# Kernel tuning notes

Measured on AMD Instinct MI355X. Metric: run time of the kernel, lower is better.

The kernel has to match this reference:

```python
import jax, jax.numpy as jnp
import numpy as np

H = 1024        # hidden_size
E = 8           # num_experts
K = 2           # top_k
FF = 4 * H      # expert hidden dim
B, S = 2, 2048


def setup_inputs() -> dict:
    key = jax.random.key(0)
    ks = jax.random.split(key, 7)
    scale = 0.02
    x = jax.random.normal(ks[0], (B, S, H), dtype=jnp.float32)
    Wg = jax.random.normal(ks[1], (H, E), dtype=jnp.float32) * scale
    bg = jnp.zeros((E,), dtype=jnp.float32)
    W1 = jax.random.normal(ks[2], (E, H, FF), dtype=jnp.float32) * scale
    b1 = jnp.zeros((E, FF), dtype=jnp.float32)
    W2 = jax.random.normal(ks[3], (E, FF, H), dtype=jnp.float32) * scale
    b2 = jnp.zeros((E, H), dtype=jnp.float32)
    return {"x": x, "Wg": Wg, "bg": bg, "W1": W1, "b1": b1, "W2": W2, "b2": b2}


def reference(x, Wg, bg, W1, b1, W2, b2):
    b, s, h = x.shape
    xf = x.reshape(-1, h)                                  # [T, H]
    T = xf.shape[0]
    # gating: softmax -> top-k -> renormalize
    probs = jax.nn.softmax(xf @ Wg + bg, axis=-1)          # [T, E]
    vals, idx = jax.lax.top_k(probs, K)                    # [T, K]
    vals = vals / jnp.sum(vals, axis=-1, keepdims=True)
    # dense combine weights: zero for non-selected experts (equivalent math)
    combine = jnp.zeros((T, E), dtype=x.dtype)
    combine = combine.at[jnp.arange(T)[:, None], idx].set(vals)  # [T, E]
    # all-expert FFN (GEMM-dominated), combined with sparse gate weights
    hmid = jax.nn.gelu(jnp.einsum('th,ehf->tef', xf, W1) + b1, approximate=False)  # [T,E,FF]
    y = jnp.einsum('tef,efh->teh', hmid, W2) + b2          # [T, E, H]
    out = jnp.einsum('te,teh->th', combine, y)             # [T, H]
    return out.reshape(b, s, h)
```

## Files before the change

### kernel.cpp

```cpp
#include <hip/hip_runtime.h>
#include <hip/hip_bf16.h>
#include <math.h>

#define T_TOK  4096
#define H_DIM  1024
#define E_NUM  8
#define FF_DIM 4096
#define KSEL   2
#define SLOTS  (T_TOK*KSEL)
#define SLOTS_PAD (SLOTS + 256)
#define BM 128
#define MAXTILES 72

typedef __attribute__((ext_vector_type(8))) short s16x8;
typedef __attribute__((ext_vector_type(8))) unsigned short u16x8;
typedef __attribute__((ext_vector_type(4))) float f32x4;

typedef __attribute__((address_space(1))) const void global_cvoid;
typedef __attribute__((address_space(3))) void lds_void;

__device__ __forceinline__ unsigned short f2bf(float f){
  unsigned int u = __float_as_uint(f);
  u += 0x7fffu + ((u>>16)&1u);
  return (unsigned short)(u>>16);
}
__device__ __forceinline__ float bf2f(unsigned short h){
  return __uint_as_float(((unsigned int)h)<<16);
}

static constexpr size_t OFF_CNT   = 0;
static constexpr size_t OFF_IDX   = 1280;
static constexpr size_t OFF_POS   = OFF_IDX  + 32768;
static constexpr size_t OFF_WV    = OFF_POS  + 32768;
static constexpr size_t OFF_SLOT  = OFF_WV   + 32768;
static constexpr size_t OFF_WOF   = OFF_SLOT + 32768;
static constexpr size_t OFF_XG    = OFF_WOF  + 32768;
static constexpr size_t OFF_W1T   = OFF_XG  + (size_t)SLOTS_PAD*H_DIM*2;
static constexpr size_t OFF_W2T   = OFF_W1T + (size_t)E_NUM*H_DIM*FF_DIM*2;
static constexpr size_t OFF_MID   = OFF_W2T + (size_t)E_NUM*H_DIM*FF_DIM*2;
static constexpr size_t OFF_Y     = OFF_MID + (size_t)SLOTS_PAD*FF_DIM*2;

__global__ __launch_bounds__(256) void prep_kernel(
    const float* __restrict__ W1, unsigned short* __restrict__ W1t,
    const float* __restrict__ W2, unsigned short* __restrict__ W2t,
    const float* __restrict__ x, const float* __restrict__ Wg,
    const float* __restrict__ bg, int* __restrict__ cnt,
    int* __restrict__ idxp, int* __restrict__ posp, float* __restrict__ wvp)
{
  int id = blockIdx.x;
  if (id < 256){
    int lane = threadIdx.x & 63;
    int wv = threadIdx.x >> 6;
    for (int tt=0; tt<4; ++tt){
      int t = (id*4 + wv)*4 + tt;
      const float* xr = x + (size_t)t*H_DIM;
      float acc[E_NUM];
      #pragma unroll
      for (int e=0;e<E_NUM;e++) acc[e]=0.f;
      for (int i=0;i<H_DIM/64;i++){
        int h = i*64 + lane;
        float xv = xr[h];
        const float* wr_ = Wg + (size_t)h*E_NUM;
        #pragma unroll
        for (int e=0;e<E_NUM;e++) acc[e] += xv*wr_[e];
      }
      #pragma unroll
      for (int e=0;e<E_NUM;e++){
        #pragma unroll
        for (int off=32; off>0; off>>=1) acc[e] += __shfl_xor(acc[e], off);
      }
      if (lane==0){
        float l[E_NUM];
        #pragma unroll
        for (int e=0;e<E_NUM;e++) l[e] = acc[e] + bg[e];
        int i0 = 0;
        #pragma unroll
        for (int e=1;e<E_NUM;e++) if (l[e] > l[i0]) i0 = e;
        int i1 = (i0==0)?1:0;
        #pragma unroll
        for (int e=0;e<E_NUM;e++) if (e!=i0 && l[e] > l[i1]) i1 = e;
        float p1 = expf(l[i1]-l[i0]);
        float s  = 1.f + p1;
        float w0 = 1.f/s, w1 = p1/s;
        int pos0 = atomicAdd(&cnt[i0],1);
        int pos1 = atomicAdd(&cnt[i1],1);
        idxp[t*2]=i0; idxp[t*2+1]=i1;
        posp[t*2]=pos0; posp[t*2+1]=pos1;
        wvp[t*2]=w0; wvp[t*2+1]=w1;
      }
    }
    return;
  }
  __shared__ float tile[64][65];
  int id2 = id - 256;
  const float* in; unsigned short* out; int R, C, cx, cy, e;
  if (id2 < 8192){
    e = id2 >> 10; int rem = id2 & 1023;
    cx = rem & 63; cy = rem >> 6;
    R = H_DIM; C = FF_DIM; in = W1; out = W1t;
  } else {
    int id3 = id2 - 8192;
    e = id3 >> 10; int rem = id3 & 1023;
    cx = rem & 15; cy = rem >> 4;
    R = FF_DIM; C = H_DIM; in = W2; out = W2t;
  }
  const float* inp = in + (size_t)e*R*C;
  unsigned short* op = out + (size_t)e*R*C;
  int c0 = cx*64, r0 = cy*64;
  int tx = threadIdx.x & 15, ty = threadIdx.x >> 4;
  #pragma unroll
  for (int i=0;i<4;i++){
    int r = i*16 + ty;
    float4 v = *(const float4*)(inp + (size_t)(r0+r)*C + c0 + tx*4);
    tile[r][tx*4+0]=v.x; tile[r][tx*4+1]=v.y; tile[r][tx*4+2]=v.z; tile[r][tx*4+3]=v.w;
  }
  __syncthreads();
  int wx = threadIdx.x & 7;
  int wcl = threadIdx.x >> 3;
  #pragma unroll
  for (int i=0;i<2;i++){
    int c = i*32 + wcl;
    u16x8 o;
    #pragma unroll
    for (int j=0;j<8;j++) o[j] = f2bf(tile[wx*8+j][c]);
    *(u16x8*)(op + (size_t)(c0+c)*R + r0 + wx*8) = o;
  }
}

__global__ __launch_bounds__(256) void route_gather_kernel(
    const float* __restrict__ x, const int* __restrict__ idxp,
    const int* __restrict__ posp, const float* __restrict__ wvp,
    const int* __restrict__ cnt,
    unsigned short* __restrict__ Xg, float* __restrict__ w_of,
    int* __restrict__ slot_of)
{
  int b = blockIdx.x;
  int t = b>>1;
  int e = idxp[b];
  int off = 0;
  #pragma unroll
  for (int i=0;i<E_NUM;i++) off += (i<e) ? cnt[i] : 0;
  int slot = off + posp[b];
  const float4* src = (const float4*)(x + (size_t)t*H_DIM);
  float4 v = src[threadIdx.x];
  ushort4 o;
  o.x=f2bf(v.x); o.y=f2bf(v.y); o.z=f2bf(v.z); o.w=f2bf(v.w);
  ((ushort4*)(Xg + (size_t)slot*H_DIM))[threadIdx.x] = o;
  if (threadIdx.x == 0){
    w_of[slot] = wvp[b];
    slot_of[b] = slot;
  }
}

#define GLDS(g, l) __builtin_amdgcn_global_load_lds((global_cvoid*)(g), (lds_void*)(l), 16, 0, 0)

template<int MODE>
__global__ __launch_bounds__(256, 4) void gemm128_kernel(
    const unsigned short* __restrict__ A,
    const unsigned short* __restrict__ Bt,
    const float* __restrict__ bias,
    unsigned short* __restrict__ Out,
    const int* __restrict__ cnt,
    const float* __restrict__ w_of,
    int N, int K, int cpcs)
{
  int L = blockIdx.x;
  int xcd = L & 7;
  int slot = L >> 3;
  int within = slot & 15;
  int chunk = ((slot >> 4) << 3) + xcd;
  int tb = chunk >> cpcs;
  int cb = chunk & ((1<<cpcs)-1);
  int tile_id = tb*4 + (within & 3);
  int col0 = (cb*4 + (within >> 2)) << 7;

  int e=0, row0=0, nv=0, acc_t=0, o=0, found=0;
  #pragma unroll
  for (int i=0;i<E_NUM;i++){
    int c = cnt[i];
    int nt = (c + BM-1) >> 7;
    if (!found && tile_id < acc_t + nt){
      int mt = tile_id - acc_t;
      e = i; row0 = o + mt*BM; nv = c - mt*BM; found = 1;
    }
    acc_t += nt; o += c;
  }
  if (!found) return;
  int nvalid = nv > BM ? BM : nv;
  const unsigned short* Be = Bt + (size_t)e*N*K;

  __shared__ unsigned short As[2][128*32];
  __shared__ unsigned short Bs[2][128*32];
  char* asb = (char*)&As[0][0];
  char* bsb = (char*)&Bs[0][0];

  int t = threadIdx.x;
  int wid = t>>6, lane = t&63;
  int wr = (wid>>1)*64, wc = (wid&1)*64;
  int fr = lane&15, fq = lane>>4;

  int srow = t>>2;
  int scl  = ((t&3) - ((t>>3)&3)) & 3;
  int sdst = wid*1024;

  const unsigned short* pA0 = A  + (size_t)(row0 + srow)*K      + scl*8;
  const unsigned short* pA1 = A  + (size_t)(row0 + 64 + srow)*K + scl*8;
  const unsigned short* pB0 = Be + (size_t)(col0 + srow)*K      + scl*8;
  const unsigned short* pB1 = Be + (size_t)(col0 + 64 + srow)*K + scl*8;

  auto stage = [&](int buf, int kelem){
    GLDS(pA0 + kelem, asb + buf*8192 + sdst);
    GLDS(pA1 + kelem, asb + buf*8192 + 4096 + sdst);
    GLDS(pB0 + kelem, bsb + buf*8192 + sdst);
    GLDS(pB1 + kelem, bsb + buf*8192 + 4096 + sdst);
  };

  int rd_sw = ((fq + ((fr>>1)&3)) & 3) << 4;

  f32x4 acc[4][4];
  #pragma unroll
  for (int i=0;i<4;i++)
    #pragma unroll
    for (int j=0;j<4;j++) acc[i][j] = (f32x4){0.f,0.f,0.f,0.f};

  int NT = K >> 5;
  stage(0, 0);
  stage(1, 32);
  for (int kt=0; kt<NT; ++kt){
    int cur = kt&1;
    if (kt+1 < NT) asm volatile("s_waitcnt vmcnt(4)" ::: "memory");
    else           asm volatile("s_waitcnt vmcnt(0)" ::: "memory");
    __builtin_amdgcn_s_barrier();
    asm volatile("" ::: "memory");

    s16x8 af[4], bfr[4];
    #pragma unroll
    for (int i=0;i<4;i++){
      af[i]  = *(const s16x8*)(asb + cur*8192 + (wr + i*16 + fr)*64 + rd_sw);
      bfr[i] = *(const s16x8*)(bsb + cur*8192 + (wc + i*16 + fr)*64 + rd_sw);
    }
    #pragma unroll
    for (int i=0;i<4;i++)
      #pragma unroll
      for (int j=0;j<4;j++)
        acc[i][j] = __builtin_amdgcn_mfma_f32_16x16x32_bf16(af[i], bfr[j], acc[i][j], 0,0,0);

    asm volatile("s_waitcnt lgkmcnt(0)" ::: "memory");
    __builtin_amdgcn_s_barrier();
    asm volatile("" ::: "memory");
    if (kt+2 < NT) stage(cur, (kt+2)*32);
  }

  float bias_v[4];
  #pragma unroll
  for (int j=0;j<4;j++) bias_v[j] = bias[(size_t)e*N + col0 + wc + j*16 + fr];
  #pragma unroll
  for (int i=0;i<4;i++){
    #pragma unroll
    for (int r=0;r<4;r++){
      int lrow = wr + i*16 + fq*4 + r;
      if (lrow < nvalid){
        int grow = row0 + lrow;
        float scale = (MODE==1) ? w_of[grow] : 0.f;
        #pragma unroll
        for (int j=0;j<4;j++){
          int col = col0 + wc + j*16 + fr;
          float v = acc[i][j][r] + bias_v[j];
          if (MODE==0){
            float u = v*(0.7978845608f + 0.0356774081f*v*v);
            float z = __expf(2.f*u);
            v = v - __fdividef(v, z + 1.f);
          } else {
            v *= scale;
          }
          Out[(size_t)grow*N + col] = f2bf(v);
        }
      }
    }
  }
}

__global__ __launch_bounds__(256) void combine_kernel(
    const unsigned short* __restrict__ y, const int* __restrict__ slot_of,
    float* __restrict__ out)
{
  int tok = blockIdx.x;
  int s0 = slot_of[tok*2], s1 = slot_of[tok*2+1];
  const ushort4* y0 = (const ushort4*)(y + (size_t)s0*H_DIM);
  const ushort4* y1 = (const ushort4*)(y + (size_t)s1*H_DIM);
  float4* o = (float4*)(out + (size_t)tok*H_DIM);
  ushort4 a = y0[threadIdx.x], b = y1[threadIdx.x];
  float4 r;
  r.x = bf2f(a.x)+bf2f(b.x);
  r.y = bf2f(a.y)+bf2f(b.y);
  r.z = bf2f(a.z)+bf2f(b.z);
  r.w = bf2f(a.w)+bf2f(b.w);
  o[threadIdx.x] = r;
}

extern "C" void kernel_launch(void* const* d_in, const int* in_sizes, int n_in,
                              void* d_out, int out_size, void* d_ws, size_t ws_size,
                              hipStream_t stream) {
  const float* x  = (const float*)d_in[0];
  const float* Wg = (const float*)d_in[1];
  const float* bg = (const float*)d_in[2];
  const float* W1 = (const float*)d_in[3];
  const float* b1 = (const float*)d_in[4];
  const float* W2 = (const float*)d_in[5];
  const float* b2 = (const float*)d_in[6];
  float* out = (float*)d_out;
  char* ws = (char*)d_ws;

  int*   cnt      = (int*)  (ws + OFF_CNT);
  int*   idxp     = (int*)  (ws + OFF_IDX);
  int*   posp     = (int*)  (ws + OFF_POS);
  float* wvp      = (float*)(ws + OFF_WV);
  int*   slot_of  = (int*)  (ws + OFF_SLOT);
  float* w_of     = (float*)(ws + OFF_WOF);
  unsigned short* Xg  = (unsigned short*)(ws + OFF_XG);
  unsigned short* W1t = (unsigned short*)(ws + OFF_W1T);
  unsigned short* W2t = (unsigned short*)(ws + OFF_W2T);
  unsigned short* mid = (unsigned short*)(ws + OFF_MID);
  unsigned short* y   = (unsigned short*)(ws + OFF_Y);

  hipMemsetAsync(ws + OFF_CNT, 0, 32, stream);

  prep_kernel<<<dim3(16640), 256, 0, stream>>>(
      W1, W1t, W2, W2t, x, Wg, bg, cnt, idxp, posp, wvp);
  route_gather_kernel<<<SLOTS, 256, 0, stream>>>(x, idxp, posp, wvp, cnt, Xg, w_of, slot_of);

  gemm128_kernel<0><<<dim3(2304), 256, 0, stream>>>(
      Xg, W1t, b1, mid, cnt, nullptr, FF_DIM, H_DIM, 3);
  gemm128_kernel<1><<<dim3(640), 256, 0, stream>>>(
      mid, W2t, b2, y, cnt, w_of, H_DIM, FF_DIM, 1);

  combine_kernel<<<T_TOK, 256, 0, stream>>>(y, slot_of, out);
}
```

Measured before the change: 410.9 us.

## Overlap W2 transpose-convert with first GEMM and batch transposes into prefetched strips

Measured after the change: 397.8 us. 3.2% less time.

```diff
diff --git a/kernel.cpp b/kernel.cpp
--- a/kernel.cpp
+++ b/kernel.cpp
@@ -40,13 +40,54 @@
 static constexpr size_t OFF_MID   = OFF_W2T + (size_t)E_NUM*H_DIM*FF_DIM*2;
 static constexpr size_t OFF_Y     = OFF_MID + (size_t)SLOTS_PAD*FF_DIM*2;
 
+__device__ __forceinline__ void transconv_strip(
+    const float* __restrict__ inp, unsigned short* __restrict__ op,
+    int R, int C, int r0, int c0base, char* smem)
+{
+  float (*tile)[65] = (float(*)[65])smem;
+  int tx = threadIdx.x & 15, ty = threadIdx.x >> 4;
+  int wx = threadIdx.x & 7,  wcl = threadIdx.x >> 3;
+  float4 cur[4], nxt[4];
+  #pragma unroll
+  for (int i=0;i<4;i++)
+    cur[i] = *(const float4*)(inp + (size_t)(r0+i*16+ty)*C + c0base + tx*4);
+  for (int it=0; it<4; ++it){
+    int c0 = c0base + it*64;
+    if (it < 3){
+      #pragma unroll
+      for (int i=0;i<4;i++)
+        nxt[i] = *(const float4*)(inp + (size_t)(r0+i*16+ty)*C + c0 + 64 + tx*4);
+    }
+    #pragma unroll
+    for (int i=0;i<4;i++){
+      int r = i*16 + ty;
+      tile[r][tx*4+0]=cur[i].x; tile[r][tx*4+1]=cur[i].y;
+      tile[r][tx*4+2]=cur[i].z; tile[r][tx*4+3]=cur[i].w;
+    }
+    __syncthreads();
+    #pragma unroll
+    for (int i=0;i<2;i++){
+      int c = i*32 + wcl;
+      u16x8 o;
+      #pragma unroll
+      for (int j=0;j<8;j++) o[j] = f2bf(tile[wx*8+j][c]);
+      *(u16x8*)(op + (size_t)(c0+c)*R + r0 + wx*8) = o;
+    }
+    __syncthreads();
+    if (it < 3){
+      #pragma unroll
+      for (int i=0;i<4;i++) cur[i] = nxt[i];
+    }
+  }
+}
+
 __global__ __launch_bounds__(256) void prep_kernel(
     const float* __restrict__ W1, unsigned short* __restrict__ W1t,
-    const float* __restrict__ W2, unsigned short* __restrict__ W2t,
     const float* __restrict__ x, const float* __restrict__ Wg,
     const float* __restrict__ bg, int* __restrict__ cnt,
     int* __restrict__ idxp, int* __restrict__ posp, float* __restrict__ wvp)
 {
+  __shared__ char smem[16768];
   int id = blockIdx.x;
   if (id < 256){
     int lane = threadIdx.x & 63;
@@ -91,40 +132,12 @@
     }
     return;
   }
-  __shared__ float tile[64][65];
-  int id2 = id - 256;
-  const float* in; unsigned short* out; int R, C, cx, cy, e;
-  if (id2 < 8192){
-    e = id2 >> 10; int rem = id2 & 1023;
-    cx = rem & 63; cy = rem >> 6;
-    R = H_DIM; C = FF_DIM; in = W1; out = W1t;
-  } else {
-    int id3 = id2 - 8192;
-    e = id3 >> 10; int rem = id3 & 1023;
-    cx = rem & 15; cy = rem >> 4;
-    R = FF_DIM; C = H_DIM; in = W2; out = W2t;
-  }
-  const float* inp = in + (size_t)e*R*C;
-  unsigned short* op = out + (size_t)e*R*C;
-  int c0 = cx*64, r0 = cy*64;
-  int tx = threadIdx.x & 15, ty = threadIdx.x >> 4;
-  #pragma unroll
-  for (int i=0;i<4;i++){
-    int r = i*16 + ty;
-    float4 v = *(const float4*)(inp + (size_t)(r0+r)*C + c0 + tx*4);
-    tile[r][tx*4+0]=v.x; tile[r][tx*4+1]=v.y; tile[r][tx*4+2]=v.z; tile[r][tx*4+3]=v.w;
-  }
-  __syncthreads();
-  int wx = threadIdx.x & 7;
-  int wcl = threadIdx.x >> 3;
-  #pragma unroll
-  for (int i=0;i<2;i++){
-    int c = i*32 + wcl;
-    u16x8 o;
-    #pragma unroll
-    for (int j=0;j<8;j++) o[j] = f2bf(tile[wx*8+j][c]);
-    *(u16x8*)(op + (size_t)(c0+c)*R + r0 + wx*8) = o;
-  }
+  int s = id - 256;
+  int e = s >> 8;
+  int rem = s & 255;
+  int rs = rem >> 4, cs = rem & 15;
+  transconv_strip(W1 + (size_t)e*H_DIM*FF_DIM, W1t + (size_t)e*H_DIM*FF_DIM,
+                  H_DIM, FF_DIM, rs*64, cs*256, smem);
 }
 
 __global__ __launch_bounds__(256) void route_gather_kernel(
@@ -162,11 +175,24 @@
     unsigned short* __restrict__ Out,
     const int* __restrict__ cnt,
     const float* __restrict__ w_of,
+    const float* __restrict__ Wsrc,
+    unsigned short* __restrict__ Wdst,
     int N, int K, int cpcs)
 {
+  __shared__ char smem[32768];
   int L = blockIdx.x;
-  int xcd = L & 7;
-  int slot = L >> 3;
+  if (MODE==0 && L < 2048){
+    int e = L >> 8;
+    int rem = L & 255;
+    int rs = rem >> 2, cs = rem & 3;
+    transconv_strip(Wsrc + (size_t)e*H_DIM*FF_DIM, Wdst + (size_t)e*H_DIM*FF_DIM,
+                    FF_DIM, H_DIM, rs*64, cs*256, smem);
+    return;
+  }
+  int L2 = (MODE==0) ? (L - 2048) : L;
+
+  int xcd = L2 & 7;
+  int slot = L2 >> 3;
   int within = slot & 15;
   int chunk = ((slot >> 4) << 3) + xcd;
   int tb = chunk >> cpcs;
@@ -189,10 +215,8 @@
   int nvalid = nv > BM ? BM : nv;
   const unsigned short* Be = Bt + (size_t)e*N*K;
 
-  __shared__ unsigned short As[2][128*32];
-  __shared__ unsigned short Bs[2][128*32];
-  char* asb = (char*)&As[0][0];
-  char* bsb = (char*)&Bs[0][0];
+  char* asb = smem;
+  char* bsb = smem + 16384;
 
   int t = threadIdx.x;
   int wid = t>>6, lane = t&63;
@@ -325,14 +349,14 @@
 
   hipMemsetAsync(ws + OFF_CNT, 0, 32, stream);
 
-  prep_kernel<<<dim3(16640), 256, 0, stream>>>(
-      W1, W1t, W2, W2t, x, Wg, bg, cnt, idxp, posp, wvp);
+  prep_kernel<<<dim3(2304), 256, 0, stream>>>(
+      W1, W1t, x, Wg, bg, cnt, idxp, posp, wvp);
   route_gather_kernel<<<SLOTS, 256, 0, stream>>>(x, idxp, posp, wvp, cnt, Xg, w_of, slot_of);
 
-  gemm128_kernel<0><<<dim3(2304), 256, 0, stream>>>(
-      Xg, W1t, b1, mid, cnt, nullptr, FF_DIM, H_DIM, 3);
+  gemm128_kernel<0><<<dim3(2048 + 2304), 256, 0, stream>>>(
+      Xg, W1t, b1, mid, cnt, nullptr, W2, W2t, FF_DIM, H_DIM, 3);
   gemm128_kernel<1><<<dim3(640), 256, 0, stream>>>(
-      mid, W2t, b2, y, cnt, w_of, H_DIM, FF_DIM, 1);
+      mid, W2t, b2, y, cnt, w_of, nullptr, nullptr, H_DIM, FF_DIM, 1);
 
   combine_kernel<<<T_TOK, 256, 0, stream>>>(y, slot_of, out);
 }
```
